# Kernel tuning notes

Measured on AMD Instinct MI355X. Metric: run time of the kernel, lower is better.

Reference implementation:

```python
import jax, jax.numpy as jnp
import numpy as np

MSE_W = 0.1
RANK_W = 0.9
DIV_W = 0.1
MARGIN = 0.2


def setup_inputs() -> dict:
    key = jax.random.key(0)
    k1, k2 = jax.random.split(key)
    N = 8192
    predictions = jax.random.normal(k1, (N,), dtype=jnp.float32)
    targets = jax.random.uniform(k2, (N,), dtype=jnp.float32)
    return {"predictions": predictions, "targets": targets}


def _ranking_loss(pred, tgt, margin):
    n = pred.shape[0]
    # pairwise differences [N, N]; only i<j (strict upper triangle) contributes
    dp = pred[:, None] - pred[None, :]
    dt = tgt[:, None] - tgt[None, :]
    hi = jnp.maximum(margin - dp, 0.0)      # target_diff >  margin branch
    lo = jnp.maximum(margin + dp, 0.0)      # target_diff < -margin branch
    mid = 0.1 * jnp.abs(dp)                 # |target_diff| <= margin branch
    per_pair = jnp.where(dt > margin, hi, jnp.where(dt < -margin, lo, mid))
    upper = jnp.triu(jnp.ones((n, n), dtype=jnp.bool_), k=1)
    total = jnp.sum(jnp.where(upper, per_pair, 0.0))
    pair_count = n * (n - 1) // 2
    return total / max(pair_count, 1)


def _diversity_loss(pred, tgt):
    # torch.var is unbiased (ddof=1)
    pred_var = jnp.var(pred, ddof=1)
    tgt_var = jnp.var(tgt, ddof=1)
    return jnp.maximum(tgt_var - pred_var, 0.0)


def reference(predictions, targets):
    mse = jnp.mean((predictions - targets) ** 2)
    rank = _ranking_loss(predictions, targets, MARGIN)
    div = _diversity_loss(predictions, targets)
    return MSE_W * mse + RANK_W * rank + DIV_W * div
```

## Files before the change

kernel.cpp:

```cpp
#include <hip/hip_runtime.h>

#define MSE_W  0.1
#define RANK_W 0.9
#define DIV_W  0.1
#define MARGIN 0.2f

#define BLK   256
#define RPT   4
#define ROWS  (BLK * RPT)
#define CCH   64
#define RATIO (ROWS / CCH)
#define CHUNK 16
#define NCH   (CCH / CHUNK)
#define PAD   1e30f

__device__ __forceinline__ float pair_term(float pi, float ti, float f, float g) {
    const float dp = pi - f;
    const float dt = ti - g;
    const unsigned sgn = __float_as_uint(dt) & 0x80000000u;
    const float y = __uint_as_float(__float_as_uint(dp) ^ sgn);
    const float outer = fmaxf(MARGIN - y, 0.0f);
    const float mid   = 0.1f * fabsf(dp);
    return (fabsf(dt) > MARGIN) ? outer : mid;
}

__global__ __launch_bounds__(BLK)
void pair_partials(const float* __restrict__ pred, const float* __restrict__ tgt,
                   int n, int gcols, int grows, float* __restrict__ partials) {
    __shared__ float sred[BLK / 64];
    const int tid = threadIdx.x;
    const int bid = blockIdx.x;

    int rb = 0, off = 0;
    for (; rb + 1 < grows; ++rb) {
        const int cnt = gcols - RATIO * rb;
        if (bid < off + cnt) break;
        off += cnt;
    }
    const int cb = RATIO * rb + (bid - off);
    const float w = (cb < RATIO * (rb + 1)) ? 0.5f : 1.0f;

    float pi[RPT], ti[RPT], acc[RPT];
    #pragma unroll
    for (int r = 0; r < RPT; ++r) {
        const int i = rb * ROWS + r * BLK + tid;
        pi[r] = (i < n) ? pred[i] : PAD;
        ti[r] = (i < n) ? tgt[i]  : PAD;
        acc[r] = 0.0f;
    }

    const int jbase = cb * CCH;
    if (jbase + CCH <= n) {
        const float* __restrict__ cp = pred + jbase;
        const float* __restrict__ ct = tgt  + jbase;
        float f[2][CHUNK], g[2][CHUNK];
        #pragma unroll
        for (int q = 0; q < CHUNK; ++q) { f[0][q] = cp[q]; g[0][q] = ct[q]; }
        #pragma unroll
        for (int c = 0; c < NCH; ++c) {
            const int cur = c & 1;
            if (c + 1 < NCH) {
                const int nxt = cur ^ 1;
                const int base = (c + 1) * CHUNK;
                #pragma unroll
                for (int q = 0; q < CHUNK; ++q) {
                    f[nxt][q] = cp[base + q];
                    g[nxt][q] = ct[base + q];
                }
            }
            #pragma unroll
            for (int q = 0; q < CHUNK; ++q) {
                #pragma unroll
                for (int r = 0; r < RPT; ++r)
                    acc[r] += pair_term(pi[r], ti[r], f[cur][q], g[cur][q]);
            }
        }
    } else {
        for (int s = 0; s < CCH; ++s) {
            const int j = jbase + s;
            const float fv = (j < n) ? pred[j] : PAD;
            const float gv = (j < n) ? tgt[j]  : PAD;
            #pragma unroll
            for (int r = 0; r < RPT; ++r)
                acc[r] += pair_term(pi[r], ti[r], fv, gv);
        }
    }

    float a = (acc[0] + acc[1]) + (acc[2] + acc[3]);
    #pragma unroll
    for (int offs = 32; offs > 0; offs >>= 1) a += __shfl_down(a, offs, 64);
    if ((tid & 63) == 0) sred[tid >> 6] = a;
    __syncthreads();
    if (tid == 0) {
        float s = 0.0f;
        #pragma unroll
        for (int wv = 0; wv < BLK / 64; ++wv) s += sred[wv];
        partials[bid] = s * w;
    }
}

__global__ __launch_bounds__(256)
void finalize_kernel(const float* __restrict__ pred, const float* __restrict__ tgt,
                     const float* __restrict__ partials, int nparts, int n,
                     float* __restrict__ out) {
    __shared__ float sm[6][4];
    const int tid = threadIdx.x;

    float rk = 0.0f;
    for (int i = tid; i < nparts; i += 256) rk += partials[i];

    float se = 0.f, p = 0.f, p2 = 0.f, t = 0.f, t2 = 0.f;
    for (int i = tid; i < n; i += 256) {
        const float pv = pred[i];
        const float tv = tgt[i];
        const float d  = pv - tv;
        se += d * d;
        p += pv; p2 += pv * pv;
        t += tv; t2 += tv * tv;
    }

    #pragma unroll
    for (int off = 32; off > 0; off >>= 1) {
        rk += __shfl_down(rk, off, 64);
        se += __shfl_down(se, off, 64);
        p  += __shfl_down(p,  off, 64);
        p2 += __shfl_down(p2, off, 64);
        t  += __shfl_down(t,  off, 64);
        t2 += __shfl_down(t2, off, 64);
    }
    if ((tid & 63) == 0) {
        const int w = tid >> 6;
        sm[0][w] = rk; sm[1][w] = se; sm[2][w] = p;
        sm[3][w] = p2; sm[4][w] = t;  sm[5][w] = t2;
    }
    __syncthreads();
    if (tid == 0) {
        double R = 0, SE = 0, P = 0, P2 = 0, T = 0, T2 = 0;
        for (int w = 0; w < 4; ++w) {
            R  += sm[0][w]; SE += sm[1][w]; P  += sm[2][w];
            P2 += sm[3][w]; T  += sm[4][w]; T2 += sm[5][w];
        }
        const double nn = (double)n;
        const double pair_count = nn * (nn - 1.0) * 0.5;
        const double rank  = R / pair_count;
        const double mse   = SE / nn;
        const double var_p = (P2 - P * P / nn) / (nn - 1.0);
        const double var_t = (T2 - T * T / nn) / (nn - 1.0);
        double div = var_t - var_p;
        if (div < 0.0) div = 0.0;
        out[0] = (float)(MSE_W * mse + RANK_W * rank + DIV_W * div);
    }
}

extern "C" void kernel_launch(void* const* d_in, const int* in_sizes, int n_in,
                              void* d_out, int out_size, void* d_ws, size_t ws_size,
                              hipStream_t stream) {
    const float* pred = (const float*)d_in[0];
    const float* tgt  = (const float*)d_in[1];
    const int n = in_sizes[0];
    float* ws  = (float*)d_ws;
    float* out = (float*)d_out;

    const int gcols = (n + CCH - 1) / CCH;
    const int grows = (n + ROWS - 1) / ROWS;
    int nblocks = 0;
    for (int rb = 0; rb < grows; ++rb) {
        const int cnt = gcols - RATIO * rb;
        nblocks += (cnt > 0) ? cnt : 0;
    }

    pair_partials<<<nblocks, BLK, 0, stream>>>(pred, tgt, n, gcols, grows, ws);
    finalize_kernel<<<1, 256, 0, stream>>>(pred, tgt, ws, nblocks, n, out);
}
```

Measured before the change: 71.83 us.

## Use one row per thread and move moment reduction into pair kernel block 0

Each thread now handles a single row instead of four, so row blocks are 256 tall and the grid gets roughly four times as many blocks, each doing less work. The MSE and variance moment sums move out of the single-block finalize kernel into block 0 of the pair kernel, so they overlap with the pairwise work and finalize only reduces partials. This trades register-level reuse of each column load across four rows for more parallelism, and adds more partials, more column loads and a longer tail for block 0.

New measurement: 66.27 us. -7.7%, faster.

```diff
diff --git a/kernel.cpp b/kernel.cpp
--- a/kernel.cpp
+++ b/kernel.cpp
@@ -6,8 +6,7 @@
 #define MARGIN 0.2f
 
 #define BLK   256
-#define RPT   4
-#define ROWS  (BLK * RPT)
+#define ROWS  256
 #define CCH   64
 #define RATIO (ROWS / CCH)
 #define CHUNK 16
@@ -26,28 +25,26 @@
 
 __global__ __launch_bounds__(BLK)
 void pair_partials(const float* __restrict__ pred, const float* __restrict__ tgt,
-                   int n, int gcols, int grows, float* __restrict__ partials) {
+                   int n, int gcols, int grows, float* __restrict__ partials,
+                   int nparts) {
     __shared__ float sred[BLK / 64];
     const int tid = threadIdx.x;
     const int bid = blockIdx.x;
 
     int rb = 0, off = 0;
     for (; rb + 1 < grows; ++rb) {
-        const int cnt = gcols - RATIO * rb;
+        int cnt = gcols - RATIO * rb;
+        if (cnt < 0) cnt = 0;
         if (bid < off + cnt) break;
         off += cnt;
     }
     const int cb = RATIO * rb + (bid - off);
     const float w = (cb < RATIO * (rb + 1)) ? 0.5f : 1.0f;
 
-    float pi[RPT], ti[RPT], acc[RPT];
-    #pragma unroll
-    for (int r = 0; r < RPT; ++r) {
-        const int i = rb * ROWS + r * BLK + tid;
-        pi[r] = (i < n) ? pred[i] : PAD;
-        ti[r] = (i < n) ? tgt[i]  : PAD;
-        acc[r] = 0.0f;
-    }
+    const int i = rb * ROWS + tid;
+    const float pi = (i < n) ? pred[i] : PAD;
+    const float ti = (i < n) ? tgt[i]  : PAD;
+    float acc0 = 0.0f, acc1 = 0.0f;
 
     const int jbase = cb * CCH;
     if (jbase + CCH <= n) {
@@ -69,10 +66,9 @@
                 }
             }
             #pragma unroll
-            for (int q = 0; q < CHUNK; ++q) {
-                #pragma unroll
-                for (int r = 0; r < RPT; ++r)
-                    acc[r] += pair_term(pi[r], ti[r], f[cur][q], g[cur][q]);
+            for (int q = 0; q < CHUNK; q += 2) {
+                acc0 += pair_term(pi, ti, f[cur][q],     g[cur][q]);
+                acc1 += pair_term(pi, ti, f[cur][q + 1], g[cur][q + 1]);
             }
         }
     } else {
@@ -80,13 +76,11 @@
             const int j = jbase + s;
             const float fv = (j < n) ? pred[j] : PAD;
             const float gv = (j < n) ? tgt[j]  : PAD;
-            #pragma unroll
-            for (int r = 0; r < RPT; ++r)
-                acc[r] += pair_term(pi[r], ti[r], fv, gv);
+            acc0 += pair_term(pi, ti, fv, gv);
         }
     }
 
-    float a = (acc[0] + acc[1]) + (acc[2] + acc[3]);
+    float a = acc0 + acc1;
     #pragma unroll
     for (int offs = 32; offs > 0; offs >>= 1) a += __shfl_down(a, offs, 64);
     if ((tid & 63) == 0) sred[tid >> 6] = a;
@@ -97,49 +91,65 @@
         for (int wv = 0; wv < BLK / 64; ++wv) s += sred[wv];
         partials[bid] = s * w;
     }
+
+    if (bid == 0) {
+        __shared__ float smom[5][BLK / 64];
+        float se = 0.f, p = 0.f, p2 = 0.f, t = 0.f, t2 = 0.f;
+        for (int k = tid; k < n; k += BLK) {
+            const float pv = pred[k];
+            const float tv = tgt[k];
+            const float d  = pv - tv;
+            se += d * d;
+            p += pv; p2 += pv * pv;
+            t += tv; t2 += tv * tv;
+        }
+        #pragma unroll
+        for (int offs = 32; offs > 0; offs >>= 1) {
+            se += __shfl_down(se, offs, 64);
+            p  += __shfl_down(p,  offs, 64);
+            p2 += __shfl_down(p2, offs, 64);
+            t  += __shfl_down(t,  offs, 64);
+            t2 += __shfl_down(t2, offs, 64);
+        }
+        if ((tid & 63) == 0) {
+            const int wv = tid >> 6;
+            smom[0][wv] = se; smom[1][wv] = p; smom[2][wv] = p2;
+            smom[3][wv] = t;  smom[4][wv] = t2;
+        }
+        __syncthreads();
+        if (tid == 0) {
+            #pragma unroll
+            for (int k = 0; k < 5; ++k) {
+                float s = 0.0f;
+                #pragma unroll
+                for (int wv = 0; wv < BLK / 64; ++wv) s += smom[k][wv];
+                partials[nparts + k] = s;
+            }
+        }
+    }
 }
 
 __global__ __launch_bounds__(256)
-void finalize_kernel(const float* __restrict__ pred, const float* __restrict__ tgt,
-                     const float* __restrict__ partials, int nparts, int n,
+void finalize_kernel(const float* __restrict__ partials, int nparts, int n,
                      float* __restrict__ out) {
-    __shared__ float sm[6][4];
+    __shared__ float sm[4];
     const int tid = threadIdx.x;
 
     float rk = 0.0f;
     for (int i = tid; i < nparts; i += 256) rk += partials[i];
-
-    float se = 0.f, p = 0.f, p2 = 0.f, t = 0.f, t2 = 0.f;
-    for (int i = tid; i < n; i += 256) {
-        const float pv = pred[i];
-        const float tv = tgt[i];
-        const float d  = pv - tv;
-        se += d * d;
-        p += pv; p2 += pv * pv;
-        t += tv; t2 += tv * tv;
-    }
-
     #pragma unroll
-    for (int off = 32; off > 0; off >>= 1) {
-        rk += __shfl_down(rk, off, 64);
-        se += __shfl_down(se, off, 64);
-        p  += __shfl_down(p,  off, 64);
-        p2 += __shfl_down(p2, off, 64);
-        t  += __shfl_down(t,  off, 64);
-        t2 += __shfl_down(t2, off, 64);
-    }
-    if ((tid & 63) == 0) {
-        const int w = tid >> 6;
-        sm[0][w] = rk; sm[1][w] = se; sm[2][w] = p;
-        sm[3][w] = p2; sm[4][w] = t;  sm[5][w] = t2;
-    }
+    for (int off = 32; off > 0; off >>= 1) rk += __shfl_down(rk, off, 64);
+    if ((tid & 63) == 0) sm[tid >> 6] = rk;
     __syncthreads();
     if (tid == 0) {
-        double R = 0, SE = 0, P = 0, P2 = 0, T = 0, T2 = 0;
-        for (int w = 0; w < 4; ++w) {
-            R  += sm[0][w]; SE += sm[1][w]; P  += sm[2][w];
-            P2 += sm[3][w]; T  += sm[4][w]; T2 += sm[5][w];
-        }
+        double R = 0;
+        #pragma unroll
+        for (int wv = 0; wv < 4; ++wv) R += sm[wv];
+        const double SE = partials[nparts + 0];
+        const double P  = partials[nparts + 1];
+        const double P2 = partials[nparts + 2];
+        const double T  = partials[nparts + 3];
+        const double T2 = partials[nparts + 4];
         const double nn = (double)n;
         const double pair_count = nn * (nn - 1.0) * 0.5;
         const double rank  = R / pair_count;
@@ -169,6 +179,6 @@
         nblocks += (cnt > 0) ? cnt : 0;
     }
 
-    pair_partials<<<nblocks, BLK, 0, stream>>>(pred, tgt, n, gcols, grows, ws);
-    finalize_kernel<<<1, 256, 0, stream>>>(pred, tgt, ws, nblocks, n, out);
+    pair_partials<<<nblocks, BLK, 0, stream>>>(pred, tgt, n, gcols, grows, ws, nblocks);
+    finalize_kernel<<<1, 256, 0, stream>>>(ws, nblocks, n, out);
 }
```
